# Kernel optimization log

Hardware: AMD Instinct MI355X
Metric: run time of the kernel (lower is better)

## Reference

```python
import jax, jax.numpy as jnp
import numpy as np

SLOT_DIM = 64
EPS_SHIFT = 1e-6


def _mlp(x, Ws, bs):
    for i in range(len(Ws) - 1):
        x = jax.nn.relu(x @ Ws[i] + bs[i])
    return x @ Ws[-1] + bs[-1]


def setup_inputs() -> dict:
    key = jax.random.key(0)
    ks = jax.random.split(key, 16)
    B, C, H, W = 2, 64, 64, 64
    Q = 65536  # 256x256 output queries
    feat = jax.random.normal(ks[0], (B, C, H, W), jnp.float32)
    coord = jax.random.uniform(ks[1], (B, Q, 2), jnp.float32, -1.0, 1.0)
    cell = jnp.full((B, Q, 2), 2.0 / 256.0, jnp.float32)
    in_dim = C * 9 + 2 + 2  # unfolded feat + rel_coord + rel_cell
    dims = [in_dim, 256, 256, 256, 256, 3]
    params = {}
    for i in range(5):
        params[f"W{i}"] = jax.random.normal(ks[2 + i], (dims[i], dims[i + 1]), jnp.float32) * (1.0 / np.sqrt(dims[i]))
        params[f"b{i}"] = jnp.zeros((dims[i + 1],), jnp.float32)
    return {"feat": feat, "coord": coord, "cell": cell, **params}


def reference(feat, coord, cell, W0, b0, W1, b1, W2, b2, W3, b3, W4, b4):
    Ws = [W0, W1, W2, W3, W4]
    bs = [b0, b1, b2, b3, b4]
    B, C, H, W = feat.shape
    slot_flat = feat[:, -SLOT_DIM:].reshape(B, SLOT_DIM, H * W)
    # F.unfold(feat, 3, padding=1): channel order c*9 + ky*3 + kx
    pad = jnp.pad(feat, ((0, 0), (0, 0), (1, 1), (1, 1)))
    feat_unf = jnp.stack(
        [pad[:, :, ky:ky + H, kx:kx + W] for ky in range(3) for kx in range(3)],
        axis=2).reshape(B, C * 9, H * W)
    rx = 1.0 / H  # 2/H/2
    ry = 1.0 / W
    preds, slots = [], []
    for vx in (-1.0, 1.0):
        for vy in (-1.0, 1.0):
            cy = jnp.clip(coord[..., 0] + vx * rx + EPS_SHIFT, -1 + 1e-6, 1 - 1e-6)
            cx = jnp.clip(coord[..., 1] + vy * ry + EPS_SHIFT, -1 + 1e-6, 1 - 1e-6)
            # nearest grid_sample, align_corners=False: pix = (c+1)*N/2 - 0.5
            iy = jnp.clip(jnp.round((cy + 1.0) * H / 2.0 - 0.5), 0, H - 1).astype(jnp.int32)
            ix = jnp.clip(jnp.round((cx + 1.0) * W / 2.0 - 0.5), 0, W - 1).astype(jnp.int32)
            idx = iy * W + ix  # [B, Q]
            q_feat = jnp.take_along_axis(feat_unf, idx[:, None, :], axis=2).transpose(0, 2, 1)  # [B,Q,C*9]
            q_slot = jnp.take_along_axis(slot_flat, idx[:, None, :], axis=2).transpose(0, 2, 1)  # [B,Q,S]
            # make_coord pixel centers at sampled indices
            qc_y = -1.0 + (2.0 * iy.astype(coord.dtype) + 1.0) / H
            qc_x = -1.0 + (2.0 * ix.astype(coord.dtype) + 1.0) / W
            rel_y = (coord[..., 0] - qc_y) * H
            rel_x = (coord[..., 1] - qc_x) * W
            rel_cell = cell * jnp.asarray([H, W], coord.dtype)
            inp = jnp.concatenate([q_feat, rel_y[..., None], rel_x[..., None], rel_cell], axis=-1)
            preds.append(_mlp(inp, Ws, bs))  # [B,Q,3]
            slots.append(q_slot)
    # self-attention ensemble weighting
    slots = jnp.stack(slots, axis=-1)  # [B,Q,S,4]
    normed = slots / jnp.linalg.norm(slots, axis=-2, keepdims=True)
    n_shift = slots.shape[-1]
    attn = jnp.einsum('bqsi,bqsj->bqij', normed, normed) / SLOT_DIM  # mean over slot dim
    mask = 1.0 - jnp.eye(n_shift, dtype=attn.dtype)
    w = jnp.mean(attn * mask[None, None], axis=-1)  # [B,Q,4]
    w = w / jnp.sum(w, axis=-1, keepdims=True)
    ret = preds[0] * w[..., 0:1]
    for i in range(1, n_shift):
        ret = ret + preds[i] * w[..., i:i + 1]
    return ret
```

## Files before the change

kernel.cpp:

```cpp
#include <hip/hip_runtime.h>
#include <hip/hip_bf16.h>
#include <hip/hip_fp16.h>

typedef _Float16 f16x8 __attribute__((ext_vector_type(8)));
typedef float f32x4 __attribute__((ext_vector_type(4)));

#define OFF_FEAT_T   0u
#define OFF_FEAT_H   (2u*1024*1024)
#define OFF_G        (3u*1024*1024)
#define OFF_WP1      (7u*1024*1024)
#define OFF_WP2      (OFF_WP1 + 131072u)
#define OFF_WP3      (OFF_WP2 + 131072u)
#define OFF_WP4      (OFF_WP3 + 131072u)
#define OFF_W0PT     (OFF_WP4 + 8192u)

__device__ __forceinline__ unsigned short f2h(float v) {
  return __builtin_bit_cast(unsigned short, (_Float16)v);
}
__device__ __forceinline__ float h2f(unsigned short u) {
  return (float)__builtin_bit_cast(_Float16, u);
}
__device__ __forceinline__ unsigned pk2(float a, float b) {
  auto p = __builtin_amdgcn_cvt_pkrtz(a, b);
  return __builtin_bit_cast(unsigned, p);
}

__global__ __launch_bounds__(256) void prep_kernel(
    const float* __restrict__ feat, const float* __restrict__ W0,
    const float* __restrict__ W1, const float* __restrict__ W2,
    const float* __restrict__ W3, const float* __restrict__ W4,
    char* __restrict__ ws)
{
  int flat = blockIdx.x * 256 + threadIdx.x;
  if (flat < 524288) {
    int c = flat & 63, x = (flat >> 6) & 63, y = (flat >> 12) & 63, b = flat >> 18;
    float f = feat[(((b*64 + c) << 6) + y)*64 + x];
    ((float*)(ws + OFF_FEAT_T))[flat] = f;
    ((unsigned short*)(ws + OFF_FEAT_H))[flat] = f2h(f);
    return;
  }
  int e = flat - 524288;
  if (e >= 43520) return;
  unsigned short o[8];
  char* dst;
  if (e < 24576) {
    int layer = e >> 13, ee = e & 8191;
    const float* Wsrc = layer == 0 ? W1 : (layer == 1 ? W2 : W3);
    int lane = ee & 63, nb = (ee >> 6) & 15, kk = ee >> 10;
    int n = nb*16 + (lane & 15), kb = kk*32 + ((lane >> 4) << 3);
    #pragma unroll
    for (int j = 0; j < 8; ++j) o[j] = f2h(Wsrc[(kb + j)*256 + n]);
    dst = ws + OFF_WP1 + layer*131072 + ee*16;
  } else if (e < 25088) {
    int ee = e - 24576;
    int lane = ee & 63, kk = ee >> 6;
    int n = lane & 15, kb = kk*32 + ((lane >> 4) << 3);
    #pragma unroll
    for (int j = 0; j < 8; ++j)
      o[j] = (n < 3) ? f2h(W4[(kb + j)*3 + n]) : (unsigned short)0;
    dst = ws + OFF_WP4 + ee*16;
  } else {
    int ee = e - 25088;
    int lane = ee & 63, nb = (ee >> 6) & 15, kk = ee >> 10;
    int n = nb*16 + (lane & 15), kb = kk*32 + ((lane >> 4) << 3);
    #pragma unroll
    for (int j = 0; j < 8; ++j) {
      int kp = kb + j, tap = kp >> 6, ch = kp & 63;
      o[j] = f2h(W0[(ch*9 + tap)*256 + n]);
    }
    dst = ws + OFF_W0PT + ee*16;
  }
  uint4 v;
  v.x = (unsigned)o[0] | ((unsigned)o[1] << 16);
  v.y = (unsigned)o[2] | ((unsigned)o[3] << 16);
  v.z = (unsigned)o[4] | ((unsigned)o[5] << 16);
  v.w = (unsigned)o[6] | ((unsigned)o[7] << 16);
  *(uint4*)dst = v;
}

__global__ __launch_bounds__(256) void g_kernel(char* __restrict__ ws)
{
  __shared__ __align__(16) char As[32 * 1152];
  int t = threadIdx.x, lane = t & 63, w = t >> 6;
  int bid = blockIdx.x, b = bid >> 7, rb = bid & 127;
  int y = rb >> 1, x0 = (rb & 1) << 5;
  {
    int r = t >> 3, cq = t & 7;
    const unsigned short* fh = (const unsigned short*)(ws + OFF_FEAT_H);
    #pragma unroll
    for (int tap = 0; tap < 9; ++tap) {
      int dy = tap/3 - 1, dx = tap%3 - 1;
      int sy = y + dy, sx = x0 + r + dx;
      uint4 v = {0,0,0,0};
      if (sy >= 0 && sy < 64 && sx >= 0 && sx < 64)
        v = *(const uint4*)(fh + (((((b << 6) + sy) << 6) + sx) << 6) + (cq << 3));
      *(uint4*)(As + r*1152 + ((tap*128 + cq*16) ^ ((r & 7) << 4))) = v;
    }
  }
  __syncthreads();
  const f32x4 vzero = {0.f, 0.f, 0.f, 0.f};
  f32x4 acc[4][2];
  #pragma unroll
  for (int i = 0; i < 4; ++i)
    #pragma unroll
    for (int j = 0; j < 2; ++j) acc[i][j] = vzero;
  const unsigned short* wp0 = (const unsigned short*)(ws + OFF_W0PT);
  int lr = lane & 15, lg = lane >> 4;
  #pragma unroll
  for (int kk = 0; kk < 18; ++kk) {
    f16x8 a[4], bf[2];
    #pragma unroll
    for (int mf = 0; mf < 4; ++mf)
      a[mf] = *(const f16x8*)(wp0 + (((kk*16 + w*4 + mf)*64 + lane) << 3));
    #pragma unroll
    for (int nf = 0; nf < 2; ++nf) {
      int row = nf*16 + lr;
      bf[nf] = *(const f16x8*)(As + row*1152 + ((kk*64 + (lg << 4)) ^ ((row & 7) << 4)));
    }
    #pragma unroll
    for (int mf = 0; mf < 4; ++mf)
      #pragma unroll
      for (int nf = 0; nf < 2; ++nf)
        acc[mf][nf] = __builtin_amdgcn_mfma_f32_16x16x32_f16(a[mf], bf[nf], acc[mf][nf], 0, 0, 0);
  }
  unsigned short* gp = (unsigned short*)(ws + OFF_G);
  #pragma unroll
  for (int mf = 0; mf < 4; ++mf)
    #pragma unroll
    for (int nf = 0; nf < 2; ++nf) {
      int col = (w << 6) + mf*16 + (lg << 2);
      int p = (y << 6) + x0 + nf*16 + lr;
      uint2 ov;
      ov.x = pk2(acc[mf][nf][0], acc[mf][nf][1]);
      ov.y = pk2(acc[mf][nf][2], acc[mf][nf][3]);
      *(uint2*)(gp + ((((b << 12) + p) << 8) + col)) = ov;
    }
}

__device__ __forceinline__ void hidden_layer(const char* src, char* dst,
                                             const unsigned short* wp,
                                             const float* bias,
                                             int lane, int wc)
{
  const f32x4 vzero = {0.f, 0.f, 0.f, 0.f};
  f32x4 acc[4][4];
  #pragma unroll
  for (int i = 0; i < 4; ++i)
    #pragma unroll
    for (int j = 0; j < 4; ++j) acc[i][j] = vzero;
  int lr = lane & 15, lg = lane >> 4;
  #pragma unroll
  for (int kk = 0; kk < 8; ++kk) {
    f16x8 a[4], bb[4];
    #pragma unroll
    for (int mf = 0; mf < 4; ++mf)
      a[mf] = *(const f16x8*)(wp + (((kk*16 + wc*4 + mf)*64 + lane) << 3));
    #pragma unroll
    for (int nf = 0; nf < 4; ++nf) {
      int row = (nf << 4) + lr;
      bb[nf] = *(const f16x8*)(src + row*512 + ((((kk << 2) + lg) ^ (row & 31)) << 4));
    }
    #pragma unroll
    for (int mf = 0; mf < 4; ++mf)
      #pragma unroll
      for (int nf = 0; nf < 4; ++nf)
        acc[mf][nf] = __builtin_amdgcn_mfma_f32_16x16x32_f16(a[mf], bb[nf], acc[mf][nf], 0, 0, 0);
  }
  #pragma unroll
  for (int mf = 0; mf < 4; ++mf) {
    int col0 = (wc << 6) + (mf << 4) + (lg << 2);
    float4 bv = *(const float4*)(bias + col0);
    int unit = (wc << 3) + (mf << 1) + (lg >> 1);
    int half8 = (lg & 1) << 3;
    #pragma unroll
    for (int nf = 0; nf < 4; ++nf) {
      int row = (nf << 4) + lr;
      float v0 = fmaxf(acc[mf][nf][0] + bv.x, 0.f);
      float v1 = fmaxf(acc[mf][nf][1] + bv.y, 0.f);
      float v2 = fmaxf(acc[mf][nf][2] + bv.z, 0.f);
      float v3 = fmaxf(acc[mf][nf][3] + bv.w, 0.f);
      uint2 ov;
      ov.x = pk2(v0, v1);
      ov.y = pk2(v2, v3);
      *(uint2*)(dst + row*512 + (((unit ^ (row & 31)) << 4) + half8)) = ov;
    }
  }
}

__global__ __launch_bounds__(256) void main_kernel(
    const float* __restrict__ coord, const float* __restrict__ cell,
    const float* __restrict__ W0, const float* __restrict__ b0,
    const float* __restrict__ b1, const float* __restrict__ b2,
    const float* __restrict__ b3, const float* __restrict__ b4,
    const char* __restrict__ ws, float* __restrict__ out)
{
  __shared__ __align__(16) char bufA[64*512];
  __shared__ __align__(16) char bufB[64*512];
  __shared__ __align__(16) float rel4[64][4];
  __shared__ int prow[64];
  __shared__ float preds[64][4];
  __shared__ float dots[16][12];

  int t = threadIdx.x, lane = t & 63, w = t >> 6;
  int bid = blockIdx.x, b = bid >> 12, qt = bid & 4095;
  int qbase = qt << 4;

  if (t < 64) {
    int r = t, ql = r >> 2, s = r & 3;
    int gq = (b << 16) + qbase + ql;
    float c0 = coord[gq*2], c1 = coord[gq*2 + 1];
    float ce0 = cell[gq*2], ce1 = cell[gq*2 + 1];
    float vx = (s & 2) ? 1.0f : -1.0f;
    float vy = (s & 1) ? 1.0f : -1.0f;
    float cy = fminf(fmaxf(c0 + vx*(1.0f/64.0f) + 1e-6f, -1.0f + 1e-6f), 1.0f - 1e-6f);
    float cx = fminf(fmaxf(c1 + vy*(1.0f/64.0f) + 1e-6f, -1.0f + 1e-6f), 1.0f - 1e-6f);
    int iy = (int)fminf(fmaxf(rintf((cy + 1.0f)*32.0f - 0.5f), 0.0f), 63.0f);
    int ix = (int)fminf(fmaxf(rintf((cx + 1.0f)*32.0f - 0.5f), 0.0f), 63.0f);
    prow[r] = (iy << 6) + ix;
    float qcy = -1.0f + (float)(2*iy + 1)*(1.0f/64.0f);
    float qcx = -1.0f + (float)(2*ix + 1)*(1.0f/64.0f);
    rel4[r][0] = (c0 - qcy)*64.0f;
    rel4[r][1] = (c1 - qcx)*64.0f;
    rel4[r][2] = ce0*64.0f;
    rel4[r][3] = ce1*64.0f;
  }
  __syncthreads();
  {
    int r = t & 63;
    int ug = __builtin_amdgcn_readfirstlane(t >> 6);
    float4 rf = *(const float4*)rel4[r];
    const unsigned short* gp = (const unsigned short*)(ws + OFF_G)
                             + (((b << 12) + prow[r]) << 8);
    int rs = r & 31;
    #pragma unroll
    for (int u = 0; u < 8; ++u) {
      int unit = u*4 + ug;
      uint4 gv = *(const uint4*)(gp + (unit << 3));
      int cb = unit << 3;
      float c0[8], c1[8], c2[8], c3[8], c4[8];
      #pragma unroll
      for (int j = 0; j < 8; ++j) {
        c0[j] = W0[576*256 + cb + j];
        c1[j] = W0[577*256 + cb + j];
        c2[j] = W0[578*256 + cb + j];
        c3[j] = W0[579*256 + cb + j];
        c4[j] = b0[cb + j];
      }
      unsigned short us[8] = {
        (unsigned short)(gv.x & 0xffff), (unsigned short)(gv.x >> 16),
        (unsigned short)(gv.y & 0xffff), (unsigned short)(gv.y >> 16),
        (unsigned short)(gv.z & 0xffff), (unsigned short)(gv.z >> 16),
        (unsigned short)(gv.w & 0xffff), (unsigned short)(gv.w >> 16) };
      float hv[8];
      #pragma unroll
      for (int j = 0; j < 8; ++j) {
        float h = fmaf(rf.x, c0[j],
                  fmaf(rf.y, c1[j],
                  fmaf(rf.z, c2[j],
                  fmaf(rf.w, c3[j], h2f(us[j]) + c4[j]))));
        hv[j] = fmaxf(h, 0.0f);
      }
      uint4 ov;
      ov.x = pk2(hv[0], hv[1]);
      ov.y = pk2(hv[2], hv[3]);
      ov.z = pk2(hv[4], hv[5]);
      ov.w = pk2(hv[6], hv[7]);
      *(uint4*)(bufA + r*512 + ((unit ^ rs) << 4)) = ov;
    }
  }
  __syncthreads();
  hidden_layer(bufA, bufB, (const unsigned short*)(ws + OFF_WP1), b1, lane, w);
  __syncthreads();
  hidden_layer(bufB, bufA, (const unsigned short*)(ws + OFF_WP2), b2, lane, w);
  __syncthreads();
  hidden_layer(bufA, bufB, (const unsigned short*)(ws + OFF_WP3), b3, lane, w);
  __syncthreads();
  {
    const unsigned short* wp4 = (const unsigned short*)(ws + OFF_WP4);
    const f32x4 vzero = {0.f, 0.f, 0.f, 0.f};
    f32x4 acc = vzero;
    int lr = lane & 15, lg = lane >> 4;
    int row = (w << 4) + lr;
    #pragma unroll
    for (int kk = 0; kk < 8; ++kk) {
      f16x8 a = *(const f16x8*)(wp4 + ((kk*64 + lane) << 3));
      f16x8 bb = *(const f16x8*)(bufB + row*512 + ((((kk << 2) + lg) ^ (row & 31)) << 4));
      acc = __builtin_amdgcn_mfma_f32_16x16x32_f16(a, bb, acc, 0, 0, 0);
    }
    if (lg == 0) {
      #pragma unroll
      for (int ch = 0; ch < 3; ++ch) preds[row][ch] = acc[ch] + b4[ch];
    }
  }
  {
    int r = t >> 2, q4 = t & 3;
    const float* sp = (const float*)(ws + OFF_FEAT_T)
                    + (((b << 12) + prow[r]) << 6) + (q4 << 4);
    float* Sld = (float*)bufA;
    #pragma unroll
    for (int i = 0; i < 4; ++i)
      *(float4*)(Sld + r*76 + (q4 << 4) + (i << 2)) = *(const float4*)(sp + (i << 2));
  }
  __syncthreads();
  if (t < 160) {
    const int ia[10] = {0,1,2,3, 0,0,0,1,1,2};
    const int ib[10] = {0,1,2,3, 1,2,3,2,3,3};
    int q = t / 10, item = t - q*10;
    const float* Sld = (const float*)bufA;
    const float* ra = Sld + (q*4 + ia[item])*76;
    const float* rb = Sld + (q*4 + ib[item])*76;
    float s = 0.0f;
    #pragma unroll
    for (int i = 0; i < 16; ++i) {
      float4 va = *(const float4*)(ra + (i << 2));
      float4 vb = *(const float4*)(rb + (i << 2));
      s += va.x*vb.x + va.y*vb.y + va.z*vb.z + va.w*vb.w;
    }
    dots[q][item] = s;
  }
  __syncthreads();
  if (t < 16) {
    int q = t;
    float inv[4];
    #pragma unroll
    for (int i = 0; i < 4; ++i) inv[i] = 1.0f / sqrtf(dots[q][i]);
    const int pa[6] = {0,0,0,1,1,2};
    const int pb[6] = {1,2,3,2,3,3};
    float wgt[4] = {0.f, 0.f, 0.f, 0.f};
    #pragma unroll
    for (int pi = 0; pi < 6; ++pi) {
      float cij = dots[q][4 + pi]*inv[pa[pi]]*inv[pb[pi]];
      wgt[pa[pi]] += cij;
      wgt[pb[pi]] += cij;
    }
    float wsum = wgt[0] + wgt[1] + wgt[2] + wgt[3];
    float invw = 1.0f / wsum;
    size_t obase = (size_t)((b << 16) + qbase + q)*3;
    #pragma unroll
    for (int cch = 0; cch < 3; ++cch) {
      float v = preds[q*4 + 0][cch]*wgt[0] + preds[q*4 + 1][cch]*wgt[1]
              + preds[q*4 + 2][cch]*wgt[2] + preds[q*4 + 3][cch]*wgt[3];
      out[obase + cch] = v*invw;
    }
  }
}

extern "C" void kernel_launch(void* const* d_in, const int* in_sizes, int n_in,
                              void* d_out, int out_size, void* d_ws, size_t ws_size,
                              hipStream_t stream) {
  const float* feat  = (const float*)d_in[0];
  const float* coord = (const float*)d_in[1];
  const float* cell  = (const float*)d_in[2];
  const float* W0 = (const float*)d_in[3];
  const float* b0 = (const float*)d_in[4];
  const float* W1 = (const float*)d_in[5];
  const float* b1 = (const float*)d_in[6];
  const float* W2 = (const float*)d_in[7];
  const float* b2 = (const float*)d_in[8];
  const float* W3 = (const float*)d_in[9];
  const float* b3 = (const float*)d_in[10];
  const float* W4 = (const float*)d_in[11];
  const float* b4 = (const float*)d_in[12];
  char* ws = (char*)d_ws;
  float* out = (float*)d_out;
  prep_kernel<<<2218, 256, 0, stream>>>(feat, W0, W1, W2, W3, W4, ws);
  g_kernel<<<256, 256, 0, stream>>>(ws);
  main_kernel<<<8192, 256, 0, stream>>>(coord, cell, W0, b0, b1, b2, b3, b4, ws, out);
}
```

Measured before the change: 352.7 us.

## Compute first-layer coord/cell/bias term via MFMA and prefetch per-layer weights

Moves the rel_coord/rel_cell/bias contribution of layer 0 from scalar FMAs over global W0 loads into a single MFMA using a packed fp16 extension weight block built in prep. It adds the precomputed gather term G in packed half arithmetic, folds biases into accumulator initialisation for the hidden layers, and prefetches the first k-slice of each layer's weights before the barrier. It also replaces __syncthreads with a lighter waitcnt+s_barrier. The layer-0 sum is now done in fp16 instead of fp32, which reduces precision, and the lighter barrier does not wait on outstanding global stores.

```diff
diff --git a/kernel.cpp b/kernel.cpp
--- a/kernel.cpp
+++ b/kernel.cpp
@@ -3,6 +3,7 @@
 #include <hip/hip_fp16.h>
 
 typedef _Float16 f16x8 __attribute__((ext_vector_type(8)));
+typedef _Float16 h2 __attribute__((ext_vector_type(2)));
 typedef float f32x4 __attribute__((ext_vector_type(4)));
 
 #define OFF_FEAT_T   0u
@@ -13,20 +14,23 @@
 #define OFF_WP3      (OFF_WP2 + 131072u)
 #define OFF_WP4      (OFF_WP3 + 131072u)
 #define OFF_W0PT     (OFF_WP4 + 8192u)
+#define OFF_W0E      (OFF_W0PT + 294912u)
 
 __device__ __forceinline__ unsigned short f2h(float v) {
   return __builtin_bit_cast(unsigned short, (_Float16)v);
-}
-__device__ __forceinline__ float h2f(unsigned short u) {
-  return (float)__builtin_bit_cast(_Float16, u);
 }
 __device__ __forceinline__ unsigned pk2(float a, float b) {
   auto p = __builtin_amdgcn_cvt_pkrtz(a, b);
   return __builtin_bit_cast(unsigned, p);
 }
+__device__ __forceinline__ void block_sync() {
+  asm volatile("s_waitcnt lgkmcnt(0)" ::: "memory");
+  __builtin_amdgcn_s_barrier();
+}
 
 __global__ __launch_bounds__(256) void prep_kernel(
     const float* __restrict__ feat, const float* __restrict__ W0,
+    const float* __restrict__ b0,
     const float* __restrict__ W1, const float* __restrict__ W2,
     const float* __restrict__ W3, const float* __restrict__ W4,
     char* __restrict__ ws)
@@ -40,7 +44,7 @@
     return;
   }
   int e = flat - 524288;
-  if (e >= 43520) return;
+  if (e >= 44544) return;
   unsigned short o[8];
   char* dst;
   if (e < 24576) {
@@ -59,7 +63,7 @@
     for (int j = 0; j < 8; ++j)
       o[j] = (n < 3) ? f2h(W4[(kb + j)*3 + n]) : (unsigned short)0;
     dst = ws + OFF_WP4 + ee*16;
-  } else {
+  } else if (e < 43520) {
     int ee = e - 25088;
     int lane = ee & 63, nb = (ee >> 6) & 15, kk = ee >> 10;
     int n = nb*16 + (lane & 15), kb = kk*32 + ((lane >> 4) << 3);
@@ -69,6 +73,17 @@
       o[j] = f2h(W0[(ch*9 + tap)*256 + n]);
     }
     dst = ws + OFF_W0PT + ee*16;
+  } else {
+    int ee = e - 43520;
+    int lane = ee & 63, nb = ee >> 6;
+    int n = nb*16 + (lane & 15), kb = (lane >> 4) << 3;
+    #pragma unroll
+    for (int j = 0; j < 8; ++j) {
+      int k = kb + j;
+      float v = (k < 4) ? W0[(576 + k)*256 + n] : (k == 4 ? b0[n] : 0.0f);
+      o[j] = f2h(v);
+    }
+    dst = ws + OFF_W0E + ee*16;
   }
   uint4 v;
   v.x = (unsigned)o[0] | ((unsigned)o[1] << 16);
@@ -140,21 +155,25 @@
 __device__ __forceinline__ void hidden_layer(const char* src, char* dst,
                                              const unsigned short* wp,
                                              const float* bias,
-                                             int lane, int wc)
+                                             int lane, int wc,
+                                             const f16x8* apre)
 {
-  const f32x4 vzero = {0.f, 0.f, 0.f, 0.f};
+  int lr = lane & 15, lg = lane >> 4;
   f32x4 acc[4][4];
   #pragma unroll
-  for (int i = 0; i < 4; ++i)
-    #pragma unroll
-    for (int j = 0; j < 4; ++j) acc[i][j] = vzero;
-  int lr = lane & 15, lg = lane >> 4;
+  for (int mf = 0; mf < 4; ++mf) {
+    float4 bv = *(const float4*)(bias + (wc << 6) + (mf << 4) + (lg << 2));
+    f32x4 bi = {bv.x, bv.y, bv.z, bv.w};
+    #pragma unroll
+    for (int nf = 0; nf < 4; ++nf) acc[mf][nf] = bi;
+  }
   #pragma unroll
   for (int kk = 0; kk < 8; ++kk) {
     f16x8 a[4], bb[4];
     #pragma unroll
     for (int mf = 0; mf < 4; ++mf)
-      a[mf] = *(const f16x8*)(wp + (((kk*16 + wc*4 + mf)*64 + lane) << 3));
+      a[mf] = (kk == 0) ? apre[mf]
+            : *(const f16x8*)(wp + (((kk*16 + wc*4 + mf)*64 + lane) << 3));
     #pragma unroll
     for (int nf = 0; nf < 4; ++nf) {
       int row = (nf << 4) + lr;
@@ -168,17 +187,15 @@
   }
   #pragma unroll
   for (int mf = 0; mf < 4; ++mf) {
-    int col0 = (wc << 6) + (mf << 4) + (lg << 2);
-    float4 bv = *(const float4*)(bias + col0);
     int unit = (wc << 3) + (mf << 1) + (lg >> 1);
     int half8 = (lg & 1) << 3;
     #pragma unroll
     for (int nf = 0; nf < 4; ++nf) {
       int row = (nf << 4) + lr;
-      float v0 = fmaxf(acc[mf][nf][0] + bv.x, 0.f);
-      float v1 = fmaxf(acc[mf][nf][1] + bv.y, 0.f);
-      float v2 = fmaxf(acc[mf][nf][2] + bv.z, 0.f);
-      float v3 = fmaxf(acc[mf][nf][3] + bv.w, 0.f);
+      float v0 = fmaxf(acc[mf][nf][0], 0.f);
+      float v1 = fmaxf(acc[mf][nf][1], 0.f);
+      float v2 = fmaxf(acc[mf][nf][2], 0.f);
+      float v3 = fmaxf(acc[mf][nf][3], 0.f);
       uint2 ov;
       ov.x = pk2(v0, v1);
       ov.y = pk2(v2, v3);
@@ -189,7 +206,6 @@
 
 __global__ __launch_bounds__(256) void main_kernel(
     const float* __restrict__ coord, const float* __restrict__ cell,
-    const float* __restrict__ W0, const float* __restrict__ b0,
     const float* __restrict__ b1, const float* __restrict__ b2,
     const float* __restrict__ b3, const float* __restrict__ b4,
     const char* __restrict__ ws, float* __restrict__ out)
@@ -202,9 +218,17 @@
   __shared__ float dots[16][12];
 
   int t = threadIdx.x, lane = t & 63, w = t >> 6;
+  int lr = lane & 15, lg = lane >> 4;
   int bid = blockIdx.x, b = bid >> 12, qt = bid & 4095;
   int qbase = qt << 4;
 
+  f16x8 a0[4];
+  {
+    const unsigned short* w0e = (const unsigned short*)(ws + OFF_W0E);
+    #pragma unroll
+    for (int mf = 0; mf < 4; ++mf)
+      a0[mf] = *(const f16x8*)(w0e + (((w*4 + mf)*64 + lane) << 3));
+  }
   if (t < 64) {
     int r = t, ql = r >> 2, s = r & 3;
     int gq = (b << 16) + qbase + ql;
@@ -224,62 +248,83 @@
     rel4[r][2] = ce0*64.0f;
     rel4[r][3] = ce1*64.0f;
   }
-  __syncthreads();
+  block_sync();
   {
-    int r = t & 63;
-    int ug = __builtin_amdgcn_readfirstlane(t >> 6);
-    float4 rf = *(const float4*)rel4[r];
-    const unsigned short* gp = (const unsigned short*)(ws + OFF_G)
-                             + (((b << 12) + prow[r]) << 8);
-    int rs = r & 31;
-    #pragma unroll
-    for (int u = 0; u < 8; ++u) {
-      int unit = u*4 + ug;
-      uint4 gv = *(const uint4*)(gp + (unit << 3));
-      int cb = unit << 3;
-      float c0[8], c1[8], c2[8], c3[8], c4[8];
-      #pragma unroll
-      for (int j = 0; j < 8; ++j) {
-        c0[j] = W0[576*256 + cb + j];
-        c1[j] = W0[577*256 + cb + j];
-        c2[j] = W0[578*256 + cb + j];
-        c3[j] = W0[579*256 + cb + j];
-        c4[j] = b0[cb + j];
+    f16x8 bb0[4];
+    int pr[4];
+    #pragma unroll
+    for (int nf = 0; nf < 4; ++nf) {
+      int row = (nf << 4) + lr;
+      float4 rv = *(const float4*)rel4[row];
+      pr[nf] = prow[row];
+      f16x8 v;
+      v[0] = (_Float16)rv.x; v[1] = (_Float16)rv.y;
+      v[2] = (_Float16)rv.z; v[3] = (_Float16)rv.w;
+      v[4] = (_Float16)1.0f; v[5] = (_Float16)0.0f;
+      v[6] = (_Float16)0.0f; v[7] = (_Float16)0.0f;
+      bb0[nf] = v;
+    }
+    const unsigned short* gtab = (const unsigned short*)(ws + OFF_G);
+    uint2 gg[4][4];
+    #pragma unroll
+    for (int nf = 0; nf < 4; ++nf) {
+      const unsigned short* gpn = gtab + (((b << 12) + pr[nf]) << 8) + (w << 6) + (lg << 2);
+      #pragma unroll
+      for (int mf = 0; mf < 4; ++mf)
+        gg[mf][nf] = *(const uint2*)(gpn + (mf << 4));
+    }
+    const f32x4 vzero = {0.f, 0.f, 0.f, 0.f};
+    f32x4 acc[4][4];
+    #pragma unroll
+    for (int mf = 0; mf < 4; ++mf)
+      #pragma unroll
+      for (int nf = 0; nf < 4; ++nf)
+        acc[mf][nf] = __builtin_amdgcn_mfma_f32_16x16x32_f16(a0[mf], bb0[nf], vzero, 0, 0, 0);
+    const h2 z2 = {(_Float16)0.0f, (_Float16)0.0f};
+    #pragma unroll
+    for (int mf = 0; mf < 4; ++mf) {
+      int unit = (w << 3) + (mf << 1) + (lg >> 1);
+      int half8 = (lg & 1) << 3;
+      #pragma unroll
+      for (int nf = 0; nf < 4; ++nf) {
+        int row = (nf << 4) + lr;
+        h2 p0 = __builtin_bit_cast(h2, pk2(acc[mf][nf][0], acc[mf][nf][1]));
+        h2 p1 = __builtin_bit_cast(h2, pk2(acc[mf][nf][2], acc[mf][nf][3]));
+        h2 g0 = __builtin_bit_cast(h2, gg[mf][nf].x);
+        h2 g1 = __builtin_bit_cast(h2, gg[mf][nf].y);
+        h2 h0 = __builtin_elementwise_max(p0 + g0, z2);
+        h2 h1 = __builtin_elementwise_max(p1 + g1, z2);
+        uint2 ov;
+        ov.x = __builtin_bit_cast(unsigned, h0);
+        ov.y = __builtin_bit_cast(unsigned, h1);
+        *(uint2*)(bufA + row*512 + (((unit ^ (row & 31)) << 4) + half8)) = ov;
       }
-      unsigned short us[8] = {
-        (unsigned short)(gv.x & 0xffff), (unsigned short)(gv.x >> 16),
-        (unsigned short)(gv.y & 0xffff), (unsigned short)(gv.y >> 16),
-        (unsigned short)(gv.z & 0xffff), (unsigned short)(gv.z >> 16),
-        (unsigned short)(gv.w & 0xffff), (unsigned short)(gv.w >> 16) };
-      float hv[8];
-      #pragma unroll
-      for (int j = 0; j < 8; ++j) {
-        float h = fmaf(rf.x, c0[j],
-                  fmaf(rf.y, c1[j],
-                  fmaf(rf.z, c2[j],
-                  fmaf(rf.w, c3[j], h2f(us[j]) + c4[j]))));
-        hv[j] = fmaxf(h, 0.0f);
-      }
-      uint4 ov;
-      ov.x = pk2(hv[0], hv[1]);
-      ov.y = pk2(hv[2], hv[3]);
-      ov.z = pk2(hv[4], hv[5]);
-      ov.w = pk2(hv[6], hv[7]);
-      *(uint4*)(bufA + r*512 + ((unit ^ rs) << 4)) = ov;
-    }
-  }
-  __syncthreads();
-  hidden_layer(bufA, bufB, (const unsigned short*)(ws + OFF_WP1), b1, lane, w);
-  __syncthreads();
-  hidden_layer(bufB, bufA, (const unsigned short*)(ws + OFF_WP2), b2, lane, w);
-  __syncthreads();
-  hidden_layer(bufA, bufB, (const unsigned short*)(ws + OFF_WP3), b3, lane, w);
-  __syncthreads();
+    }
+  }
+  const unsigned short* wp1 = (const unsigned short*)(ws + OFF_WP1);
+  const unsigned short* wp2 = (const unsigned short*)(ws + OFF_WP2);
+  const unsigned short* wp3 = (const unsigned short*)(ws + OFF_WP3);
+  f16x8 ap[4];
+  #pragma unroll
+  for (int mf = 0; mf < 4; ++mf)
+    ap[mf] = *(const f16x8*)(wp1 + (((w*4 + mf)*64 + lane) << 3));
+  block_sync();
+  hidden_layer(bufA, bufB, wp1, b1, lane, w, ap);
+  #pragma unroll
+  for (int mf = 0; mf < 4; ++mf)
+    ap[mf] = *(const f16x8*)(wp2 + (((w*4 + mf)*64 + lane) << 3));
+  block_sync();
+  hidden_layer(bufB, bufA, wp2, b2, lane, w, ap);
+  #pragma unroll
+  for (int mf = 0; mf < 4; ++mf)
+    ap[mf] = *(const f16x8*)(wp3 + (((w*4 + mf)*64 + lane) << 3));
+  block_sync();
+  hidden_layer(bufA, bufB, wp3, b3, lane, w, ap);
+  block_sync();
   {
     const unsigned short* wp4 = (const unsigned short*)(ws + OFF_WP4);
     const f32x4 vzero = {0.f, 0.f, 0.f, 0.f};
     f32x4 acc = vzero;
-    int lr = lane & 15, lg = lane >> 4;
     int row = (w << 4) + lr;
     #pragma unroll
     for (int kk = 0; kk < 8; ++kk) {
@@ -301,7 +346,7 @@
     for (int i = 0; i < 4; ++i)
       *(float4*)(Sld + r*76 + (q4 << 4) + (i << 2)) = *(const float4*)(sp + (i << 2));
   }
-  __syncthreads();
+  block_sync();
   if (t < 160) {
     const int ia[10] = {0,1,2,3, 0,0,0,1,1,2};
     const int ib[10] = {0,1,2,3, 1,2,3,2,3,3};
@@ -318,7 +363,7 @@
     }
     dots[q][item] = s;
   }
-  __syncthreads();
+  block_sync();
   if (t < 16) {
     int q = t;
     float inv[4];
@@ -363,7 +408,7 @@
   const float* b4 = (const float*)d_in[12];
   char* ws = (char*)d_ws;
   float* out = (float*)d_out;
-  prep_kernel<<<2218, 256, 0, stream>>>(feat, W0, W1, W2, W3, W4, ws);
+  prep_kernel<<<2222, 256, 0, stream>>>(feat, W0, b0, W1, W2, W3, W4, ws);
   g_kernel<<<256, 256, 0, stream>>>(ws);
-  main_kernel<<<8192, 256, 0, stream>>>(coord, cell, W0, b0, b1, b2, b3, b4, ws, out);
-}
+  main_kernel<<<8192, 256, 0, stream>>>(coord, cell, b1, b2, b3, b4, ws, out);
+}
```

New measurement: 366.6 us. 1.04x slower.
